# Kernel tuning notes

Measured on AMD Instinct MI355X. Metric: run time of the kernel, lower is better.

Reference implementation:

```python
import jax, jax.numpy as jnp
import numpy as np

# pywt db4 decomposition filters (dec_lo, dec_hi), length 8
DB4_DEC_LO = np.array([-0.010597401784997278, 0.032883011666982945,
                       0.030841381835986965, -0.18703481171888114,
                       -0.02798376941698385, 0.6308807679295904,
                       0.7148465705525415, 0.23037781330885523], dtype=np.float32)
DB4_DEC_HI = np.array([-0.23037781330885523, 0.7148465705525415,
                       -0.6308807679295904, -0.02798376941698385,
                       0.18703481171888114, 0.030841381835986965,
                       -0.032883011666982945, -0.010597401784997278], dtype=np.float32)
LEVEL = 3


def setup_inputs() -> dict:
    key = jax.random.key(0)
    x = jax.random.normal(key, (64, 32, 4096), dtype=jnp.float32)  # (B, N, T)
    return {"x": x,
            "dec_lo": jnp.asarray(DB4_DEC_LO),
            "dec_hi": jnp.asarray(DB4_DEC_HI)}


def _swt(x, dec_lo, dec_hi, level=LEVEL):
    """Stationary (a trous) wavelet transform, matching ptwt.swt semantics."""
    B, N, T = x.shape
    filt_len = dec_lo.shape[0]
    # ptwt flips the filters so conv1d (correlation) performs true convolution
    filt = jnp.stack([dec_lo[::-1], dec_hi[::-1]], axis=0)[:, None, :]  # (2, 1, L)
    res_lo = x.reshape(B * N, 1, T)
    details = []
    for lvl in range(level):
        dil = 2 ** lvl
        padl = dil * (filt_len // 2 - 1)
        padr = dil * (filt_len // 2)
        padded = jnp.pad(res_lo, ((0, 0), (0, 0), (padl, padr)), mode="wrap")  # circular
        res = jax.lax.conv_general_dilated(
            padded, filt, window_strides=(1,), padding="VALID",
            rhs_dilation=(dil,), dimension_numbers=("NCH", "OIH", "NCH"))  # (BN, 2, T)
        res_lo = res[:, 0:1, :]
        details.append(res[:, 1, :])
    # ptwt ordering: [cA_level, cD_level, ..., cD_1]
    coeffs = [res_lo[:, 0, :]] + details[::-1]
    stacked = jnp.stack(coeffs, axis=1)  # (B*N, level+1, T)
    return stacked.reshape(B, N, level + 1, T).transpose(0, 1, 3, 2)  # (B, N, T, level+1)


def reference(x, dec_lo, dec_hi):
    return _swt(x, dec_lo, dec_hi)
```

## Files before the change

### kernel.cpp

```cpp
#include <hip/hip_runtime.h>

#define TLEN 4096
#define NT 256
#define SEG 1024
#define OFF 24
#define BUFW 2176
#define NSEGS 4

typedef float f32x4 __attribute__((ext_vector_type(4)));
typedef float f32x2 __attribute__((ext_vector_type(2)));

__device__ __forceinline__ f32x4 ldv4(const float* p) {
    return *reinterpret_cast<const f32x4*>(p);
}

#define W16(n) ((n) < 4 ? qa[(n)] : (n) < 8 ? qb[(n)-4] : (n) < 12 ? qc[(n)-8] : qd[(n)-12])
#define W20(n) ((n) < 4 ? qa[(n)] : (n) < 8 ? qb[(n)-4] : (n) < 12 ? qc[(n)-8] : (n) < 16 ? qd[(n)-12] : qe[(n)-16])
#define W32(n) ((n) < 4 ? qa[(n)] : (n) < 8 ? qb[(n)-4] : (n) < 12 ? qc[(n)-8] : (n) < 16 ? qd[(n)-12] : \
                (n) < 20 ? qe[(n)-16] : (n) < 24 ? qf[(n)-20] : (n) < 28 ? qg[(n)-24] : qh[(n)-28])

__global__ __launch_bounds__(NT) void swt_db4_l3_kernel(
    const float* __restrict__ x,
    const float* __restrict__ lo_g,
    const float* __restrict__ hi_g,
    float* __restrict__ out)
{
    __shared__ float lds[2 * BUFW];
    float* bufX = lds;
    float* bufY = lds + BUFW;
    float* pl   = lds;

    const int row = blockIdx.x;
    const int tid = threadIdx.x;

    f32x2 c[8];
#pragma unroll
    for (int j = 0; j < 8; ++j) { c[j].x = lo_g[j]; c[j].y = hi_g[j]; }

    const float* xr = x + (size_t)row * TLEN;
    f32x4* outb = reinterpret_cast<f32x4*>(out + (size_t)row * TLEN * 4);

    const int hu = (tid < 21) ? (tid - 21) : (SEG + tid - 21);

    f32x4 xpre = ldv4(xr + 4 * tid);
    float xh = (tid < 49) ? xr[hu & (TLEN - 1)] : 0.f;

    for (int s = 0; s < NSEGS; ++s) {
        *reinterpret_cast<f32x4*>(&bufX[OFF + 4 * tid]) = xpre;
        if (tid < 49) bufX[OFF + hu] = xh;
        __syncthreads();

        f32x4 xnext;
        float xhn = 0.f;
        if (s + 1 < NSEGS) {
            xnext = ldv4(xr + (s + 1) * SEG + 4 * tid);
            if (tid < 49) xhn = xr[((s + 1) * SEG + hu) & (TLEN - 1)];
        }

        float d1[4], d2[4], a3[4], d3[4];

        {
            const float* b = &bufX[OFF + 4 * tid - 4];
            f32x4 qa = ldv4(b), qb = ldv4(b + 4), qc = ldv4(b + 8), qd = ldv4(b + 12);
            f32x2 acc[4];
#pragma unroll
            for (int i = 0; i < 4; ++i) { acc[i].x = 0.f; acc[i].y = 0.f; }
#pragma unroll
            for (int j = 0; j < 8; ++j)
#pragma unroll
                for (int i = 0; i < 4; ++i) {
                    float v = W16(i + 8 - j);
                    f32x2 vv; vv.x = v; vv.y = v;
                    acc[i] = __builtin_elementwise_fma(c[j], vv, acc[i]);
                }
            f32x4 av; av.x = acc[0].x; av.y = acc[1].x; av.z = acc[2].x; av.w = acc[3].x;
            *reinterpret_cast<f32x4*>(&bufY[OFF + 4 * tid]) = av;
#pragma unroll
            for (int i = 0; i < 4; ++i) d1[i] = acc[i].y;
        }
        if (tid < 42) {
            int u = (tid < 18) ? (tid - 18) : (SEG + tid - 18);
            const float* sp = &bufX[OFF + u];
            float a = 0.f;
#pragma unroll
            for (int j = 0; j < 8; ++j) a = fmaf(c[j].x, sp[4 - j], a);
            bufY[OFF + u] = a;
        }
        __syncthreads();

        {
            const float* b = &bufY[OFF + 4 * tid - 8];
            f32x4 qa = ldv4(b), qb = ldv4(b + 4), qc = ldv4(b + 8), qd = ldv4(b + 12), qe = ldv4(b + 16);
            f32x2 acc[4];
#pragma unroll
            for (int i = 0; i < 4; ++i) { acc[i].x = 0.f; acc[i].y = 0.f; }
#pragma unroll
            for (int j = 0; j < 8; ++j)
#pragma unroll
                for (int i = 0; i < 4; ++i) {
                    float v = W20(i + 16 - 2 * j);
                    f32x2 vv; vv.x = v; vv.y = v;
                    acc[i] = __builtin_elementwise_fma(c[j], vv, acc[i]);
                }
            f32x4 av; av.x = acc[0].x; av.y = acc[1].x; av.z = acc[2].x; av.w = acc[3].x;
            *reinterpret_cast<f32x4*>(&bufX[OFF + 4 * tid]) = av;
#pragma unroll
            for (int i = 0; i < 4; ++i) d2[i] = acc[i].y;
        }
        if (tid < 28) {
            int u = (tid < 12) ? (tid - 12) : (SEG + tid - 12);
            const float* sp = &bufY[OFF + u];
            float a = 0.f;
#pragma unroll
            for (int j = 0; j < 8; ++j) a = fmaf(c[j].x, sp[(4 - j) * 2], a);
            bufX[OFF + u] = a;
        }
        __syncthreads();

        {
            const float* b = &bufX[OFF + 4 * tid - 12];
            f32x4 qa = ldv4(b),      qb = ldv4(b + 4),  qc = ldv4(b + 8),  qd = ldv4(b + 12),
                  qe = ldv4(b + 16), qf = ldv4(b + 20), qg = ldv4(b + 24), qh = ldv4(b + 28);
            f32x2 acc[4];
#pragma unroll
            for (int i = 0; i < 4; ++i) { acc[i].x = 0.f; acc[i].y = 0.f; }
#pragma unroll
            for (int j = 0; j < 8; ++j)
#pragma unroll
                for (int i = 0; i < 4; ++i) {
                    float v = W32(i + 28 - 4 * j);
                    f32x2 vv; vv.x = v; vv.y = v;
                    acc[i] = __builtin_elementwise_fma(c[j], vv, acc[i]);
                }
#pragma unroll
            for (int i = 0; i < 4; ++i) { a3[i] = acc[i].x; d3[i] = acc[i].y; }
        }
        __syncthreads();

        {
            f32x4 v0, v1, v2, v3;
            v0.x=a3[0]; v0.y=a3[1]; v0.z=a3[2]; v0.w=a3[3];
            v1.x=d3[0]; v1.y=d3[1]; v1.z=d3[2]; v1.w=d3[3];
            v2.x=d2[0]; v2.y=d2[1]; v2.z=d2[2]; v2.w=d2[3];
            v3.x=d1[0]; v3.y=d1[1]; v3.z=d1[2]; v3.w=d1[3];
            *reinterpret_cast<f32x4*>(&pl[0 * SEG + 4 * tid]) = v0;
            *reinterpret_cast<f32x4*>(&pl[1 * SEG + 4 * tid]) = v1;
            *reinterpret_cast<f32x4*>(&pl[2 * SEG + 4 * tid]) = v2;
            *reinterpret_cast<f32x4*>(&pl[3 * SEG + 4 * tid]) = v3;
        }
        __syncthreads();

        f32x4* outr = outb + s * SEG;
#pragma unroll
        for (int k = 0; k < 4; ++k) {
            int t = tid + k * NT;
            f32x4 o;
            o.x = pl[0 * SEG + t];
            o.y = pl[1 * SEG + t];
            o.z = pl[2 * SEG + t];
            o.w = pl[3 * SEG + t];
            outr[t] = o;
        }
        __syncthreads();

        xpre = xnext;
        xh = xhn;
    }
}

extern "C" void kernel_launch(void* const* d_in, const int* in_sizes, int n_in,
                              void* d_out, int out_size, void* d_ws, size_t ws_size,
                              hipStream_t stream) {
    const float* x  = (const float*)d_in[0];
    const float* lo = (const float*)d_in[1];
    const float* hi = (const float*)d_in[2];
    float* out = (float*)d_out;

    const int nblocks = 64 * 32;
    swt_db4_l3_kernel<<<dim3(nblocks), dim3(NT), 0, stream>>>(x, lo, hi, out);
}
```

Baseline: 31.77 us.

## Give output staging its own LDS buffer and defer stores to overlap next segment

Moves the transposed output staging area out of the aliased compute buffers into a dedicated LDS array. Each segment's global store now runs inside the next segment's compute, after its second barrier. This removes two barriers per segment and lets the store traffic overlap with convolution work. The __syncthreads calls are replaced by an explicit lgkmcnt wait plus s_barrier, which skips the wait on outstanding global loads. In exchange LDS use grows to about 24 KB per block, which may lower occupancy.

```diff
diff --git a/kernel.cpp b/kernel.cpp
--- a/kernel.cpp
+++ b/kernel.cpp
@@ -4,7 +4,7 @@
 #define NT 256
 #define SEG 1024
 #define OFF 24
-#define BUFW 2176
+#define BUFW 1088
 #define NSEGS 4
 
 typedef float f32x4 __attribute__((ext_vector_type(4)));
@@ -12,6 +12,11 @@
 
 __device__ __forceinline__ f32x4 ldv4(const float* p) {
     return *reinterpret_cast<const f32x4*>(p);
+}
+
+__device__ __forceinline__ void bar_lds() {
+    asm volatile("s_waitcnt lgkmcnt(0)" ::: "memory");
+    __builtin_amdgcn_s_barrier();
 }
 
 #define W16(n) ((n) < 4 ? qa[(n)] : (n) < 8 ? qb[(n)-4] : (n) < 12 ? qc[(n)-8] : qd[(n)-12])
@@ -25,10 +30,9 @@
     const float* __restrict__ hi_g,
     float* __restrict__ out)
 {
-    __shared__ float lds[2 * BUFW];
-    float* bufX = lds;
-    float* bufY = lds + BUFW;
-    float* pl   = lds;
+    __shared__ float bufX[BUFW];
+    __shared__ float bufY[BUFW];
+    __shared__ float pl[4][SEG];
 
     const int row = blockIdx.x;
     const int tid = threadIdx.x;
@@ -48,7 +52,7 @@
     for (int s = 0; s < NSEGS; ++s) {
         *reinterpret_cast<f32x4*>(&bufX[OFF + 4 * tid]) = xpre;
         if (tid < 49) bufX[OFF + hu] = xh;
-        __syncthreads();
+        bar_lds();
 
         f32x4 xnext;
         float xhn = 0.f;
@@ -86,7 +90,18 @@
             for (int j = 0; j < 8; ++j) a = fmaf(c[j].x, sp[4 - j], a);
             bufY[OFF + u] = a;
         }
-        __syncthreads();
+        bar_lds();
+
+        if (s > 0) {
+            f32x4* outr = outb + (s - 1) * SEG;
+#pragma unroll
+            for (int k = 0; k < 4; ++k) {
+                int t = tid + k * NT;
+                f32x4 o;
+                o.x = pl[0][t]; o.y = pl[1][t]; o.z = pl[2][t]; o.w = pl[3][t];
+                outr[t] = o;
+            }
+        }
 
         {
             const float* b = &bufY[OFF + 4 * tid - 8];
@@ -115,7 +130,7 @@
             for (int j = 0; j < 8; ++j) a = fmaf(c[j].x, sp[(4 - j) * 2], a);
             bufX[OFF + u] = a;
         }
-        __syncthreads();
+        bar_lds();
 
         {
             const float* b = &bufX[OFF + 4 * tid - 12];
@@ -135,7 +150,6 @@
 #pragma unroll
             for (int i = 0; i < 4; ++i) { a3[i] = acc[i].x; d3[i] = acc[i].y; }
         }
-        __syncthreads();
 
         {
             f32x4 v0, v1, v2, v3;
@@ -143,28 +157,26 @@
             v1.x=d3[0]; v1.y=d3[1]; v1.z=d3[2]; v1.w=d3[3];
             v2.x=d2[0]; v2.y=d2[1]; v2.z=d2[2]; v2.w=d2[3];
             v3.x=d1[0]; v3.y=d1[1]; v3.z=d1[2]; v3.w=d1[3];
-            *reinterpret_cast<f32x4*>(&pl[0 * SEG + 4 * tid]) = v0;
-            *reinterpret_cast<f32x4*>(&pl[1 * SEG + 4 * tid]) = v1;
-            *reinterpret_cast<f32x4*>(&pl[2 * SEG + 4 * tid]) = v2;
-            *reinterpret_cast<f32x4*>(&pl[3 * SEG + 4 * tid]) = v3;
+            *reinterpret_cast<f32x4*>(&pl[0][4 * tid]) = v0;
+            *reinterpret_cast<f32x4*>(&pl[1][4 * tid]) = v1;
+            *reinterpret_cast<f32x4*>(&pl[2][4 * tid]) = v2;
+            *reinterpret_cast<f32x4*>(&pl[3][4 * tid]) = v3;
         }
-        __syncthreads();
+        bar_lds();
 
-        f32x4* outr = outb + s * SEG;
+        xpre = xnext;
+        xh = xhn;
+    }
+
+    {
+        f32x4* outr = outb + (NSEGS - 1) * SEG;
 #pragma unroll
         for (int k = 0; k < 4; ++k) {
             int t = tid + k * NT;
             f32x4 o;
-            o.x = pl[0 * SEG + t];
-            o.y = pl[1 * SEG + t];
-            o.z = pl[2 * SEG + t];
-            o.w = pl[3 * SEG + t];
+            o.x = pl[0][t]; o.y = pl[1][t]; o.z = pl[2][t]; o.w = pl[3][t];
             outr[t] = o;
         }
-        __syncthreads();
-
-        xpre = xnext;
-        xh = xhn;
     }
 }
 
```

Result: no change. 32.38 us (+1.9%).
